# Kernel tuning notes

Hardware: AMD Instinct MI355X
Metric: run time of the kernel (lower is better)

The kernel has to match this reference:

```python
import jax, jax.numpy as jnp
import numpy as np

NUM_HEADS = 8
NUM_LEVELS = 4
NUM_POINTS = 4
EMBED = 256
HEAD_DIM = EMBED // NUM_HEADS
SPATIAL = [(100, 100), (50, 50), (25, 25), (13, 13)]  # (H, W) per level


def _bilinear_sample(val, grid):
    """torch.nn.functional.grid_sample(mode='bilinear', padding_mode='zeros', align_corners=False).
    val: [B, H, W, C], grid: [B, N, 2] with (x, y) in [-1, 1]. Returns [B, N, C]."""
    B, H, W, C = val.shape
    x = (grid[..., 0] + 1.0) * (W * 0.5) - 0.5
    y = (grid[..., 1] + 1.0) * (H * 0.5) - 0.5
    x0 = jnp.floor(x)
    y0 = jnp.floor(y)
    wx1 = x - x0
    wy1 = y - y0
    wx0 = 1.0 - wx1
    wy0 = 1.0 - wy1
    x0i = x0.astype(jnp.int32)
    y0i = y0.astype(jnp.int32)
    valf = val.reshape(B, H * W, C)

    def corner(xi, yi, w):
        valid = (xi >= 0) & (xi < W) & (yi >= 0) & (yi < H)
        idx = jnp.clip(yi, 0, H - 1) * W + jnp.clip(xi, 0, W - 1)
        v = jnp.take_along_axis(valf, idx[..., None], axis=1)  # [B, N, C]
        return v * (w * valid)[..., None]

    return (corner(x0i, y0i, wx0 * wy0) + corner(x0i + 1, y0i, wx1 * wy0)
            + corner(x0i, y0i + 1, wx0 * wy1) + corner(x0i + 1, y0i + 1, wx1 * wy1))


def setup_inputs() -> dict:
    key = jax.random.key(0)
    ks = jax.random.split(key, 12)
    bs, nq = 4, 6000
    nv = sum(h * w for h, w in SPATIAL)
    s = 0.02
    return {
        "query": jax.random.normal(ks[0], (bs, nq, EMBED), jnp.float32),
        "value": jax.random.normal(ks[1], (bs, nv, EMBED), jnp.float32),
        "reference_points": jax.random.uniform(ks[2], (bs, nq, NUM_LEVELS, 2), jnp.float32),
        "W_off": jax.random.normal(ks[3], (EMBED, NUM_HEADS * NUM_LEVELS * NUM_POINTS * 2), jnp.float32) * s,
        "b_off": jax.random.normal(ks[4], (NUM_HEADS * NUM_LEVELS * NUM_POINTS * 2,), jnp.float32),
        "W_attn": jax.random.normal(ks[5], (EMBED, NUM_HEADS * NUM_LEVELS * NUM_POINTS), jnp.float32) * s,
        "b_attn": jnp.zeros((NUM_HEADS * NUM_LEVELS * NUM_POINTS,), jnp.float32),
        "W_val": jax.random.normal(ks[6], (EMBED, EMBED), jnp.float32) * s,
        "b_val": jnp.zeros((EMBED,), jnp.float32),
        "W_out": jax.random.normal(ks[7], (EMBED, EMBED), jnp.float32) * s,
        "b_out": jnp.zeros((EMBED,), jnp.float32),
        "spatial_shapes": jnp.asarray(np.array(SPATIAL, dtype=np.int32)),
    }


def reference(query, value, reference_points, W_off, b_off, W_attn, b_attn,
              W_val, b_val, W_out, b_out, spatial_shapes):
    shapes = [(int(h), int(w)) for h, w in np.asarray(spatial_shapes)]
    bs, nq, _ = query.shape
    nv = value.shape[1]

    v = (value @ W_val + b_val).reshape(bs, nv, NUM_HEADS, HEAD_DIM)
    offsets = (query @ W_off + b_off).reshape(bs, nq, NUM_HEADS, NUM_LEVELS, NUM_POINTS, 2)
    aw = (query @ W_attn + b_attn).reshape(bs, nq, NUM_HEADS, NUM_LEVELS * NUM_POINTS)
    aw = jax.nn.softmax(aw, axis=-1).reshape(bs, nq, NUM_HEADS, NUM_LEVELS, NUM_POINTS)

    # offset normalizer is [W, H] per level
    norm = jnp.asarray([[w, h] for h, w in shapes], dtype=query.dtype)  # [L, 2]
    loc = reference_points[:, :, None, :, None, :] + offsets / norm[None, None, None, :, None, :]
    grids = 2.0 * loc - 1.0  # [bs, nq, H, L, P, 2]
    # -> [bs*H, nq*P, 2] per level
    grids = jnp.transpose(grids, (0, 2, 1, 3, 4, 5)).reshape(bs * NUM_HEADS, nq, NUM_LEVELS, NUM_POINTS, 2)

    v_bh = jnp.transpose(v, (0, 2, 1, 3)).reshape(bs * NUM_HEADS, nv, HEAD_DIM)
    sampled = []
    start = 0
    for l, (H_, W_) in enumerate(shapes):
        val_l = v_bh[:, start:start + H_ * W_].reshape(bs * NUM_HEADS, H_, W_, HEAD_DIM)
        grid_l = grids[:, :, l].reshape(bs * NUM_HEADS, nq * NUM_POINTS, 2)
        s_l = _bilinear_sample(val_l, grid_l).reshape(bs * NUM_HEADS, nq, NUM_POINTS, HEAD_DIM)
        sampled.append(s_l)
        start += H_ * W_
    sampled = jnp.stack(sampled, axis=2)  # [bs*H, nq, L, P, c]

    aw_bh = jnp.transpose(aw, (0, 2, 1, 3, 4)).reshape(bs * NUM_HEADS, nq, NUM_LEVELS, NUM_POINTS)
    out = (sampled * aw_bh[..., None]).sum(axis=(2, 3))  # [bs*H, nq, c]
    out = out.reshape(bs, NUM_HEADS, nq, HEAD_DIM).transpose(0, 2, 1, 3).reshape(bs, nq, EMBED)
    out = out @ W_out + b_out
    return out + query
```

## Files before the change

### kernel.cpp

```cpp
#include <hip/hip_runtime.h>
#include <hip/hip_bf16.h>

#define BS 4
#define NQ 6000
#define NV 13294
#define NH 8
#define HD 32
#define EMB 256
#define MV (BS * NV)
#define MQ (BS * NQ)

typedef __attribute__((ext_vector_type(8))) short short8;
typedef __attribute__((ext_vector_type(4))) float floatx4;

__device__ __constant__ float LVL_DIM[4] = {100.f, 50.f, 25.f, 13.f};

__device__ inline unsigned short bf16bits(float f) {
  __hip_bfloat16 h = __float2bfloat16(f);
  return *reinterpret_cast<unsigned short*>(&h);
}
__device__ inline float bflo(unsigned int u) { return __uint_as_float(u << 16); }
__device__ inline float bfhi(unsigned int u) { return __uint_as_float(u & 0xffff0000u); }

#define LDS_STRIDE 40

__global__ __launch_bounds__(256) void wtrans_kernel(
    const float* __restrict__ W_val, const float* __restrict__ W_off,
    const float* __restrict__ W_attn, const float* __restrict__ W_out,
    unsigned short* __restrict__ Wt_val, unsigned short* __restrict__ Wt_qcat,
    unsigned short* __restrict__ Wt_out) {
  const int b = blockIdx.x, k = threadIdx.x;
  if (b < 256) {
    Wt_val[b * EMB + k] = bf16bits(W_val[k * 256 + b]);
  } else if (b < 640) {
    const int n = b - 256;
    float v = (n < 256) ? W_off[k * 256 + n] : W_attn[k * 128 + (n - 256)];
    Wt_qcat[n * EMB + k] = bf16bits(v);
  } else {
    const int n = b - 640;
    Wt_out[n * EMB + k] = bf16bits(W_out[k * 256 + n]);
  }
}

__device__ inline void stageA_f32(const float* __restrict__ A, int M, int m0,
                                  int k0, unsigned short* lds, int tid) {
  const int r = tid >> 1, half = tid & 1;
  const int row = m0 + r;
  unsigned short* dst = lds + r * LDS_STRIDE + half * 16;
  if (row < M) {
    const float* src = A + (size_t)row * EMB + k0 + half * 16;
#pragma unroll
    for (int j = 0; j < 4; ++j) {
      float4 v = *(const float4*)(src + 4 * j);
      ushort4 u;
      u.x = bf16bits(v.x);
      u.y = bf16bits(v.y);
      u.z = bf16bits(v.z);
      u.w = bf16bits(v.w);
      *(ushort4*)(dst + 4 * j) = u;
    }
  } else {
    ushort4 z = make_ushort4(0, 0, 0, 0);
#pragma unroll
    for (int j = 0; j < 4; ++j) *(ushort4*)(dst + 4 * j) = z;
  }
}

__device__ inline void stage_bf16(const unsigned short* __restrict__ B, int M,
                                  int n0, int k0, unsigned short* lds, int tid) {
  const int r = tid >> 1, half = tid & 1;
  const int row = n0 + r;
  unsigned short* dst = lds + r * LDS_STRIDE + half * 16;
  if (row < M) {
    const unsigned short* src = B + (size_t)row * EMB + k0 + half * 16;
    uint4 v0 = *(const uint4*)(src);
    uint4 v1 = *(const uint4*)(src + 8);
    *(uint4*)(dst) = v0;
    *(uint4*)(dst + 8) = v1;
  } else {
    uint4 z = make_uint4(0, 0, 0, 0);
    *(uint4*)(dst) = z;
    *(uint4*)(dst + 8) = z;
  }
}

__device__ inline void mfma_step(const unsigned short* ldsA,
                                 const unsigned short* ldsB, int wm, int wn,
                                 int lane, floatx4 acc[4][4]) {
  const unsigned short* ap =
      ldsA + (wm * 64 + (lane & 15)) * LDS_STRIDE + (lane >> 4) * 8;
  const unsigned short* bp =
      ldsB + (wn * 64 + (lane & 15)) * LDS_STRIDE + (lane >> 4) * 8;
  short8 af[4], bfr[4];
#pragma unroll
  for (int t = 0; t < 4; ++t) {
    af[t] = *(const short8*)(ap + t * 16 * LDS_STRIDE);
    bfr[t] = *(const short8*)(bp + t * 16 * LDS_STRIDE);
  }
#pragma unroll
  for (int mt = 0; mt < 4; ++mt)
#pragma unroll
    for (int nt = 0; nt < 4; ++nt)
      acc[mt][nt] = __builtin_amdgcn_mfma_f32_16x16x32_bf16(af[mt], bfr[nt],
                                                            acc[mt][nt], 0, 0, 0);
}

__global__ __launch_bounds__(256) void vproj_kernel(
    const float* __restrict__ value, const unsigned short* __restrict__ Wt,
    const float* __restrict__ b_val, unsigned short* __restrict__ vbh) {
  __shared__ unsigned short ldsA[128 * LDS_STRIDE];
  __shared__ unsigned short ldsB[128 * LDS_STRIDE];
  const int tid = threadIdx.x, lane = tid & 63, w = tid >> 6;
  const int wm = w >> 1, wn = w & 1;
  const int chunk = blockIdx.x >> 4, i = blockIdx.x & 15;
  const int m0 = (chunk * 8 + (i & 7)) * 128;
  const int n0 = (i >> 3) * 128;
  floatx4 acc[4][4];
  const floatx4 zero = {0.f, 0.f, 0.f, 0.f};
#pragma unroll
  for (int i2 = 0; i2 < 4; i2++)
#pragma unroll
    for (int j = 0; j < 4; j++) acc[i2][j] = zero;

  for (int k0 = 0; k0 < EMB; k0 += 32) {
    stageA_f32(value, MV, m0, k0, ldsA, tid);
    stage_bf16(Wt, 256, n0, k0, ldsB, tid);
    __syncthreads();
    mfma_step(ldsA, ldsB, wm, wn, lane, acc);
    __syncthreads();
  }

  const int quad = lane >> 4, cl = lane & 15;
#pragma unroll
  for (int mt = 0; mt < 4; ++mt) {
#pragma unroll
    for (int r = 0; r < 4; ++r) {
      const int row = m0 + wm * 64 + mt * 16 + quad * 4 + r;
      if (row < MV) {
        const int b = row / NV, n = row - b * NV;
#pragma unroll
        for (int nt = 0; nt < 4; ++nt) {
          const int c = n0 + wn * 64 + nt * 16 + cl;
          const int h = c >> 5, d = c & 31;
          vbh[(((size_t)(b * NH + h)) * NV + n) * HD + d] =
              bf16bits(acc[mt][nt][r] + b_val[c]);
        }
      }
    }
  }
}

__global__ __launch_bounds__(256) void qproj_kernel(
    const float* __restrict__ query, const unsigned short* __restrict__ Wt,
    const float* __restrict__ refpts, const float* __restrict__ b_off,
    const float* __restrict__ b_attn, float* __restrict__ locbuf,
    float* __restrict__ awbuf) {
  __shared__ unsigned short ldsA[128 * LDS_STRIDE];
  __shared__ unsigned short ldsB[128 * LDS_STRIDE];
  const int tid = threadIdx.x, lane = tid & 63, w = tid >> 6;
  const int wm = w >> 1, wn = w & 1;
  const int chunk = blockIdx.x / 24, i = blockIdx.x % 24;
  const int m_idx = chunk * 8 + (i & 7);
  if (m_idx >= 188) return;
  const int m0 = m_idx * 128;
  const int n0 = (i >> 3) * 128;
  floatx4 acc[4][4];
  const floatx4 zero = {0.f, 0.f, 0.f, 0.f};
#pragma unroll
  for (int i2 = 0; i2 < 4; i2++)
#pragma unroll
    for (int j = 0; j < 4; j++) acc[i2][j] = zero;

  for (int k0 = 0; k0 < EMB; k0 += 32) {
    stageA_f32(query, MQ, m0, k0, ldsA, tid);
    stage_bf16(Wt, 384, n0, k0, ldsB, tid);
    __syncthreads();
    mfma_step(ldsA, ldsB, wm, wn, lane, acc);
    __syncthreads();
  }

  const int quad = lane >> 4, cl = lane & 15;
  if (n0 < 256) {
#pragma unroll
    for (int mt = 0; mt < 4; ++mt) {
#pragma unroll
      for (int r = 0; r < 4; ++r) {
        const int row = m0 + wm * 64 + mt * 16 + quad * 4 + r;
        if (row < MQ) {
#pragma unroll
          for (int nt = 0; nt < 4; ++nt) {
            const int c = n0 + wn * 64 + nt * 16 + cl;
            const int xy = c & 1, l = (c >> 3) & 3;
            const float dim = LVL_DIM[l];
            const float ref = refpts[(size_t)row * 8 + l * 2 + xy];
            locbuf[(size_t)row * 256 + c] =
                ref * dim + acc[mt][nt][r] + b_off[c] - 0.5f;
          }
        }
      }
    }
  } else {
#pragma unroll
    for (int mt = 0; mt < 4; ++mt) {
#pragma unroll
      for (int r = 0; r < 4; ++r) {
        const int row = m0 + wm * 64 + mt * 16 + quad * 4 + r;
        if (row < MQ) {
#pragma unroll
          for (int nt = 0; nt < 4; ++nt) {
            const int ca = wn * 64 + nt * 16 + cl;
            float v = acc[mt][nt][r] + b_attn[ca];
            float m = v;
            m = fmaxf(m, __shfl_xor(m, 1));
            m = fmaxf(m, __shfl_xor(m, 2));
            m = fmaxf(m, __shfl_xor(m, 4));
            m = fmaxf(m, __shfl_xor(m, 8));
            float e = __expf(v - m);
            float s = e;
            s += __shfl_xor(s, 1);
            s += __shfl_xor(s, 2);
            s += __shfl_xor(s, 4);
            s += __shfl_xor(s, 8);
            awbuf[(size_t)row * 128 + ca] = e / s;
          }
        }
      }
    }
  }
}

__global__ __launch_bounds__(256) void sample_kernel(
    const unsigned short* __restrict__ vbh, const float* __restrict__ locbuf,
    const float* __restrict__ awbuf, unsigned short* __restrict__ sampledb) {
  const int blk = blockIdx.x;
  const int t = blk >> 3;
  const int quarter = t / 1500;
  const int j = t - quarter * 1500;
  const int slice = (blk & 7) * 4 + quarter;
  const int h = slice & 7;
  const int w = threadIdx.x >> 6;
  const int lane = threadIdx.x & 63;
  const int row = (slice >> 3) * NQ + j * 4 + w;
  const int g = lane >> 2;
  const int d8 = lane & 3;
  const int l = g >> 2;

  const int W_ = (l < 2) ? ((l == 0) ? 100 : 50) : ((l == 2) ? 25 : 13);
  const int START = (l < 2) ? ((l == 0) ? 0 : 10000) : ((l == 2) ? 12500 : 13125);

  const float2 xy = *(const float2*)(locbuf + (size_t)row * 256 + h * 32 + g * 2);
  const float wgt = awbuf[(size_t)row * 128 + h * 16 + g];

  const float fx = floorf(xy.x), fy = floorf(xy.y);
  const int x0 = (int)fx, y0 = (int)fy;
  const float wx1 = xy.x - fx, wy1 = xy.y - fy;
  const float wx0 = 1.f - wx1, wy0 = 1.f - wy1;
  const int x0c = min(max(x0, 0), W_ - 1), x1c = min(max(x0 + 1, 0), W_ - 1);
  const int y0c = min(max(y0, 0), W_ - 1), y1c = min(max(y0 + 1, 0), W_ - 1);
  const float mx0 = ((unsigned)x0 < (unsigned)W_) ? wx0 : 0.f;
  const float mx1 = ((unsigned)(x0 + 1) < (unsigned)W_) ? wx1 : 0.f;
  const float my0 = ((unsigned)y0 < (unsigned)W_) ? wy0 : 0.f;
  const float my1 = ((unsigned)(y0 + 1) < (unsigned)W_) ? wy1 : 0.f;
  const float wy0w = wgt * my0, wy1w = wgt * my1;
  const float w00 = wy0w * mx0, w01 = wy0w * mx1;
  const float w10 = wy1w * mx0, w11 = wy1w * mx1;

  const unsigned int* base =
      (const unsigned int*)vbh + ((size_t)slice * NV + START) * 16 + d8 * 4;
  const int rb0 = y0c * W_, rb1 = y1c * W_;
  const uint4 u00 = *(const uint4*)(base + (size_t)(rb0 + x0c) * 16);
  const uint4 u01 = *(const uint4*)(base + (size_t)(rb0 + x1c) * 16);
  const uint4 u10 = *(const uint4*)(base + (size_t)(rb1 + x0c) * 16);
  const uint4 u11 = *(const uint4*)(base + (size_t)(rb1 + x1c) * 16);

  float a[8];
  const unsigned int* p00 = &u00.x;
  const unsigned int* p01 = &u01.x;
  const unsigned int* p10 = &u10.x;
  const unsigned int* p11 = &u11.x;
#pragma unroll
  for (int k = 0; k < 4; ++k) {
    a[2 * k] = w00 * bflo(p00[k]) + w01 * bflo(p01[k]) + w10 * bflo(p10[k]) +
               w11 * bflo(p11[k]);
    a[2 * k + 1] = w00 * bfhi(p00[k]) + w01 * bfhi(p01[k]) +
                   w10 * bfhi(p10[k]) + w11 * bfhi(p11[k]);
  }

#pragma unroll
  for (int k = 0; k < 8; ++k) {
    a[k] += __shfl_xor(a[k], 4);
    a[k] += __shfl_xor(a[k], 8);
    a[k] += __shfl_xor(a[k], 16);
    a[k] += __shfl_xor(a[k], 32);
  }

  if (g == 0) {
    uint4 o;
    o.x = (unsigned)bf16bits(a[0]) | ((unsigned)bf16bits(a[1]) << 16);
    o.y = (unsigned)bf16bits(a[2]) | ((unsigned)bf16bits(a[3]) << 16);
    o.z = (unsigned)bf16bits(a[4]) | ((unsigned)bf16bits(a[5]) << 16);
    o.w = (unsigned)bf16bits(a[6]) | ((unsigned)bf16bits(a[7]) << 16);
    *(uint4*)(sampledb + (size_t)row * EMB + h * 32 + d8 * 8) = o;
  }
}

__global__ __launch_bounds__(256) void oproj_kernel(
    const unsigned short* __restrict__ sampledb,
    const unsigned short* __restrict__ Wt, const float* __restrict__ b_out,
    const float* __restrict__ query, float* __restrict__ out) {
  __shared__ unsigned short ldsA[128 * LDS_STRIDE];
  __shared__ unsigned short ldsB[128 * LDS_STRIDE];
  const int tid = threadIdx.x, lane = tid & 63, w = tid >> 6;
  const int wm = w >> 1, wn = w & 1;
  const int chunk = blockIdx.x >> 4, i = blockIdx.x & 15;
  const int m_idx = chunk * 8 + (i & 7);
  if (m_idx >= 188) return;
  const int m0 = m_idx * 128;
  const int n0 = (i >> 3) * 128;
  floatx4 acc[4][4];
  const floatx4 zero = {0.f, 0.f, 0.f, 0.f};
#pragma unroll
  for (int i2 = 0; i2 < 4; i2++)
#pragma unroll
    for (int j = 0; j < 4; j++) acc[i2][j] = zero;

  for (int k0 = 0; k0 < EMB; k0 += 32) {
    stage_bf16(sampledb, MQ, m0, k0, ldsA, tid);
    stage_bf16(Wt, 256, n0, k0, ldsB, tid);
    __syncthreads();
    mfma_step(ldsA, ldsB, wm, wn, lane, acc);
    __syncthreads();
  }

  const int quad = lane >> 4, cl = lane & 15;
#pragma unroll
  for (int mt = 0; mt < 4; ++mt) {
#pragma unroll
    for (int r = 0; r < 4; ++r) {
      const int row = m0 + wm * 64 + mt * 16 + quad * 4 + r;
      if (row < MQ) {
#pragma unroll
        for (int nt = 0; nt < 4; ++nt) {
          const int c = n0 + wn * 64 + nt * 16 + cl;
          out[(size_t)row * EMB + c] =
              acc[mt][nt][r] + b_out[c] + query[(size_t)row * EMB + c];
        }
      }
    }
  }
}

extern "C" void kernel_launch(void* const* d_in, const int* in_sizes, int n_in,
                              void* d_out, int out_size, void* d_ws,
                              size_t ws_size, hipStream_t stream) {
  const float* query  = (const float*)d_in[0];
  const float* value  = (const float*)d_in[1];
  const float* refpts = (const float*)d_in[2];
  const float* W_off  = (const float*)d_in[3];
  const float* b_off  = (const float*)d_in[4];
  const float* W_attn = (const float*)d_in[5];
  const float* b_attn = (const float*)d_in[6];
  const float* W_val  = (const float*)d_in[7];
  const float* b_val  = (const float*)d_in[8];
  const float* W_out  = (const float*)d_in[9];
  const float* b_out  = (const float*)d_in[10];
  float* out = (float*)d_out;

  char* ws = (char*)d_ws;
  unsigned short* vbh = (unsigned short*)ws;
  float* locbuf = (float*)(ws + 27226112);
  float* awbuf = (float*)(ws + 51802112);
  unsigned short* sampledb = (unsigned short*)(ws + 64090112);
  unsigned short* Wt_val = (unsigned short*)(ws + 76378112);
  unsigned short* Wt_qcat = (unsigned short*)(ws + 76509184);
  unsigned short* Wt_out = (unsigned short*)(ws + 76705792);

  wtrans_kernel<<<896, 256, 0, stream>>>(W_val, W_off, W_attn, W_out, Wt_val,
                                         Wt_qcat, Wt_out);
  vproj_kernel<<<832, 256, 0, stream>>>(value, Wt_val, b_val, vbh);
  qproj_kernel<<<576, 256, 0, stream>>>(query, Wt_qcat, refpts, b_off, b_attn,
                                        locbuf, awbuf);
  sample_kernel<<<BS * NQ * NH / 4, 256, 0, stream>>>(vbh, locbuf, awbuf,
                                                      sampledb);
  oproj_kernel<<<384, 256, 0, stream>>>(sampledb, Wt_out, b_out, query, out);
}
```

Measured before the change: 262.5 us.

## Prefetch GEMM tiles into registers, merge value/query projections, pack sampling FMAs

The GEMM main loops now load the next K tile from global memory into registers while the MFMAs run on the current LDS tile, so global latency overlaps with compute. The value and query projection kernels are merged into one launch with 1408 blocks, which cuts one launch and lets both GEMMs share the GPU at once. The bilinear sampling inner loop is rewritten with 2-wide float vectors so the compiler can emit packed FMAs. Holding the prefetched tiles in registers raises register pressure, which may lower occupancy.

```diff
diff --git a/kernel.cpp b/kernel.cpp
--- a/kernel.cpp
+++ b/kernel.cpp
@@ -12,6 +12,7 @@
 
 typedef __attribute__((ext_vector_type(8))) short short8;
 typedef __attribute__((ext_vector_type(4))) float floatx4;
+typedef __attribute__((ext_vector_type(2))) float floatx2;
 
 __device__ __constant__ float LVL_DIM[4] = {100.f, 50.f, 25.f, 13.f};
 
@@ -21,6 +22,12 @@
 }
 __device__ inline float bflo(unsigned int u) { return __uint_as_float(u << 16); }
 __device__ inline float bfhi(unsigned int u) { return __uint_as_float(u & 0xffff0000u); }
+__device__ inline floatx2 unpk(unsigned int u) {
+  floatx2 r;
+  r.x = __uint_as_float(u << 16);
+  r.y = __uint_as_float(u & 0xffff0000u);
+  return r;
+}
 
 #define LDS_STRIDE 40
 
@@ -42,46 +49,51 @@
   }
 }
 
-__device__ inline void stageA_f32(const float* __restrict__ A, int M, int m0,
-                                  int k0, unsigned short* lds, int tid) {
+__device__ inline void loadA_f32(const float* __restrict__ A, int M, int m0,
+                                 int k0, int tid, float4 ra[4]) {
   const int r = tid >> 1, half = tid & 1;
   const int row = m0 + r;
-  unsigned short* dst = lds + r * LDS_STRIDE + half * 16;
   if (row < M) {
     const float* src = A + (size_t)row * EMB + k0 + half * 16;
 #pragma unroll
-    for (int j = 0; j < 4; ++j) {
-      float4 v = *(const float4*)(src + 4 * j);
-      ushort4 u;
-      u.x = bf16bits(v.x);
-      u.y = bf16bits(v.y);
-      u.z = bf16bits(v.z);
-      u.w = bf16bits(v.w);
-      *(ushort4*)(dst + 4 * j) = u;
-    }
+    for (int j = 0; j < 4; ++j) ra[j] = *(const float4*)(src + 4 * j);
   } else {
-    ushort4 z = make_ushort4(0, 0, 0, 0);
-#pragma unroll
-    for (int j = 0; j < 4; ++j) *(ushort4*)(dst + 4 * j) = z;
-  }
-}
-
-__device__ inline void stage_bf16(const unsigned short* __restrict__ B, int M,
-                                  int n0, int k0, unsigned short* lds, int tid) {
+#pragma unroll
+    for (int j = 0; j < 4; ++j) ra[j] = make_float4(0.f, 0.f, 0.f, 0.f);
+  }
+}
+__device__ inline void storeA_lds(unsigned short* lds, int tid,
+                                  const float4 ra[4]) {
+  const int r = tid >> 1, half = tid & 1;
+  unsigned short* dst = lds + r * LDS_STRIDE + half * 16;
+#pragma unroll
+  for (int j = 0; j < 4; ++j) {
+    ushort4 u;
+    u.x = bf16bits(ra[j].x);
+    u.y = bf16bits(ra[j].y);
+    u.z = bf16bits(ra[j].z);
+    u.w = bf16bits(ra[j].w);
+    *(ushort4*)(dst + 4 * j) = u;
+  }
+}
+__device__ inline void loadB_bf16(const unsigned short* __restrict__ B, int M,
+                                  int n0, int k0, int tid, uint4 rb[2]) {
   const int r = tid >> 1, half = tid & 1;
   const int row = n0 + r;
-  unsigned short* dst = lds + r * LDS_STRIDE + half * 16;
   if (row < M) {
     const unsigned short* src = B + (size_t)row * EMB + k0 + half * 16;
-    uint4 v0 = *(const uint4*)(src);
-    uint4 v1 = *(const uint4*)(src + 8);
-    *(uint4*)(dst) = v0;
-    *(uint4*)(dst + 8) = v1;
+    rb[0] = *(const uint4*)(src);
+    rb[1] = *(const uint4*)(src + 8);
   } else {
-    uint4 z = make_uint4(0, 0, 0, 0);
-    *(uint4*)(dst) = z;
-    *(uint4*)(dst + 8) = z;
-  }
+    rb[0] = rb[1] = make_uint4(0, 0, 0, 0);
+  }
+}
+__device__ inline void storeB_lds(unsigned short* lds, int tid,
+                                  const uint4 rb[2]) {
+  const int r = tid >> 1, half = tid & 1;
+  unsigned short* dst = lds + r * LDS_STRIDE + half * 16;
+  *(uint4*)(dst) = rb[0];
+  *(uint4*)(dst + 8) = rb[1];
 }
 
 __device__ inline void mfma_step(const unsigned short* ldsA,
@@ -105,53 +117,56 @@
                                                             acc[mt][nt], 0, 0, 0);
 }
 
-__global__ __launch_bounds__(256) void vproj_kernel(
-    const float* __restrict__ value, const unsigned short* __restrict__ Wt,
-    const float* __restrict__ b_val, unsigned short* __restrict__ vbh) {
-  __shared__ unsigned short ldsA[128 * LDS_STRIDE];
-  __shared__ unsigned short ldsB[128 * LDS_STRIDE];
-  const int tid = threadIdx.x, lane = tid & 63, w = tid >> 6;
-  const int wm = w >> 1, wn = w & 1;
-  const int chunk = blockIdx.x >> 4, i = blockIdx.x & 15;
-  const int m0 = (chunk * 8 + (i & 7)) * 128;
-  const int n0 = (i >> 3) * 128;
-  floatx4 acc[4][4];
-  const floatx4 zero = {0.f, 0.f, 0.f, 0.f};
-#pragma unroll
-  for (int i2 = 0; i2 < 4; i2++)
-#pragma unroll
-    for (int j = 0; j < 4; j++) acc[i2][j] = zero;
-
-  for (int k0 = 0; k0 < EMB; k0 += 32) {
-    stageA_f32(value, MV, m0, k0, ldsA, tid);
-    stage_bf16(Wt, 256, n0, k0, ldsB, tid);
+__device__ inline void gemm_loop_f32A(const float* __restrict__ A, int M,
+                                      int m0, const unsigned short* __restrict__ B,
+                                      int NB, int n0, unsigned short* ldsA,
+                                      unsigned short* ldsB, int tid, int wm,
+                                      int wn, int lane, floatx4 acc[4][4]) {
+  float4 ra[4];
+  uint4 rb[2];
+  loadA_f32(A, M, m0, 0, tid, ra);
+  loadB_bf16(B, NB, n0, 0, tid, rb);
+#pragma unroll
+  for (int k = 0; k < 8; ++k) {
+    storeA_lds(ldsA, tid, ra);
+    storeB_lds(ldsB, tid, rb);
     __syncthreads();
+    if (k < 7) {
+      loadA_f32(A, M, m0, (k + 1) * 32, tid, ra);
+      loadB_bf16(B, NB, n0, (k + 1) * 32, tid, rb);
+    }
     mfma_step(ldsA, ldsB, wm, wn, lane, acc);
     __syncthreads();
   }
-
-  const int quad = lane >> 4, cl = lane & 15;
-#pragma unroll
-  for (int mt = 0; mt < 4; ++mt) {
-#pragma unroll
-    for (int r = 0; r < 4; ++r) {
-      const int row = m0 + wm * 64 + mt * 16 + quad * 4 + r;
-      if (row < MV) {
-        const int b = row / NV, n = row - b * NV;
-#pragma unroll
-        for (int nt = 0; nt < 4; ++nt) {
-          const int c = n0 + wn * 64 + nt * 16 + cl;
-          const int h = c >> 5, d = c & 31;
-          vbh[(((size_t)(b * NH + h)) * NV + n) * HD + d] =
-              bf16bits(acc[mt][nt][r] + b_val[c]);
-        }
-      }
+}
+
+__device__ inline void gemm_loop_bf16A(const unsigned short* __restrict__ A,
+                                       int M, int m0,
+                                       const unsigned short* __restrict__ B,
+                                       int NB, int n0, unsigned short* ldsA,
+                                       unsigned short* ldsB, int tid, int wm,
+                                       int wn, int lane, floatx4 acc[4][4]) {
+  uint4 ra[2], rb[2];
+  loadB_bf16(A, M, m0, 0, tid, ra);
+  loadB_bf16(B, NB, n0, 0, tid, rb);
+#pragma unroll
+  for (int k = 0; k < 8; ++k) {
+    storeB_lds(ldsA, tid, ra);
+    storeB_lds(ldsB, tid, rb);
+    __syncthreads();
+    if (k < 7) {
+      loadB_bf16(A, M, m0, (k + 1) * 32, tid, ra);
+      loadB_bf16(B, NB, n0, (k + 1) * 32, tid, rb);
     }
-  }
-}
-
-__global__ __launch_bounds__(256) void qproj_kernel(
-    const float* __restrict__ query, const unsigned short* __restrict__ Wt,
+    mfma_step(ldsA, ldsB, wm, wn, lane, acc);
+    __syncthreads();
+  }
+}
+
+__global__ __launch_bounds__(256) void vqproj_kernel(
+    const float* __restrict__ value, const unsigned short* __restrict__ Wt_val,
+    const float* __restrict__ b_val, unsigned short* __restrict__ vbh,
+    const float* __restrict__ query, const unsigned short* __restrict__ Wt_qcat,
     const float* __restrict__ refpts, const float* __restrict__ b_off,
     const float* __restrict__ b_attn, float* __restrict__ locbuf,
     float* __restrict__ awbuf) {
@@ -159,69 +174,89 @@
   __shared__ unsigned short ldsB[128 * LDS_STRIDE];
   const int tid = threadIdx.x, lane = tid & 63, w = tid >> 6;
   const int wm = w >> 1, wn = w & 1;
-  const int chunk = blockIdx.x / 24, i = blockIdx.x % 24;
-  const int m_idx = chunk * 8 + (i & 7);
-  if (m_idx >= 188) return;
-  const int m0 = m_idx * 128;
-  const int n0 = (i >> 3) * 128;
   floatx4 acc[4][4];
   const floatx4 zero = {0.f, 0.f, 0.f, 0.f};
 #pragma unroll
   for (int i2 = 0; i2 < 4; i2++)
 #pragma unroll
     for (int j = 0; j < 4; j++) acc[i2][j] = zero;
-
-  for (int k0 = 0; k0 < EMB; k0 += 32) {
-    stageA_f32(query, MQ, m0, k0, ldsA, tid);
-    stage_bf16(Wt, 384, n0, k0, ldsB, tid);
-    __syncthreads();
-    mfma_step(ldsA, ldsB, wm, wn, lane, acc);
-    __syncthreads();
-  }
-
   const int quad = lane >> 4, cl = lane & 15;
-  if (n0 < 256) {
+
+  if (blockIdx.x < 832) {
+    const int chunk = blockIdx.x >> 4, i = blockIdx.x & 15;
+    const int m0 = (chunk * 8 + (i & 7)) * 128;
+    const int n0 = (i >> 3) * 128;
+    gemm_loop_f32A(value, MV, m0, Wt_val, 256, n0, ldsA, ldsB, tid, wm, wn,
+                   lane, acc);
 #pragma unroll
     for (int mt = 0; mt < 4; ++mt) {
 #pragma unroll
       for (int r = 0; r < 4; ++r) {
         const int row = m0 + wm * 64 + mt * 16 + quad * 4 + r;
-        if (row < MQ) {
+        if (row < MV) {
+          const int b = row / NV, n = row - b * NV;
 #pragma unroll
           for (int nt = 0; nt < 4; ++nt) {
             const int c = n0 + wn * 64 + nt * 16 + cl;
-            const int xy = c & 1, l = (c >> 3) & 3;
-            const float dim = LVL_DIM[l];
-            const float ref = refpts[(size_t)row * 8 + l * 2 + xy];
-            locbuf[(size_t)row * 256 + c] =
-                ref * dim + acc[mt][nt][r] + b_off[c] - 0.5f;
+            const int h = c >> 5, d = c & 31;
+            vbh[(((size_t)(b * NH + h)) * NV + n) * HD + d] =
+                bf16bits(acc[mt][nt][r] + b_val[c]);
           }
         }
       }
     }
   } else {
-#pragma unroll
-    for (int mt = 0; mt < 4; ++mt) {
-#pragma unroll
-      for (int r = 0; r < 4; ++r) {
-        const int row = m0 + wm * 64 + mt * 16 + quad * 4 + r;
-        if (row < MQ) {
-#pragma unroll
-          for (int nt = 0; nt < 4; ++nt) {
-            const int ca = wn * 64 + nt * 16 + cl;
-            float v = acc[mt][nt][r] + b_attn[ca];
-            float m = v;
-            m = fmaxf(m, __shfl_xor(m, 1));
-            m = fmaxf(m, __shfl_xor(m, 2));
-            m = fmaxf(m, __shfl_xor(m, 4));
-            m = fmaxf(m, __shfl_xor(m, 8));
-            float e = __expf(v - m);
-            float s = e;
-            s += __shfl_xor(s, 1);
-            s += __shfl_xor(s, 2);
-            s += __shfl_xor(s, 4);
-            s += __shfl_xor(s, 8);
-            awbuf[(size_t)row * 128 + ca] = e / s;
+    const int bid = blockIdx.x - 832;
+    const int chunk = bid / 24, i = bid % 24;
+    const int m_idx = chunk * 8 + (i & 7);
+    if (m_idx >= 188) return;
+    const int m0 = m_idx * 128;
+    const int n0 = (i >> 3) * 128;
+    gemm_loop_f32A(query, MQ, m0, Wt_qcat, 384, n0, ldsA, ldsB, tid, wm, wn,
+                   lane, acc);
+    if (n0 < 256) {
+#pragma unroll
+      for (int mt = 0; mt < 4; ++mt) {
+#pragma unroll
+        for (int r = 0; r < 4; ++r) {
+          const int row = m0 + wm * 64 + mt * 16 + quad * 4 + r;
+          if (row < MQ) {
+#pragma unroll
+            for (int nt = 0; nt < 4; ++nt) {
+              const int c = n0 + wn * 64 + nt * 16 + cl;
+              const int xy = c & 1, l = (c >> 3) & 3;
+              const float dim = LVL_DIM[l];
+              const float ref = refpts[(size_t)row * 8 + l * 2 + xy];
+              locbuf[(size_t)row * 256 + c] =
+                  ref * dim + acc[mt][nt][r] + b_off[c] - 0.5f;
+            }
+          }
+        }
+      }
+    } else {
+#pragma unroll
+      for (int mt = 0; mt < 4; ++mt) {
+#pragma unroll
+        for (int r = 0; r < 4; ++r) {
+          const int row = m0 + wm * 64 + mt * 16 + quad * 4 + r;
+          if (row < MQ) {
+#pragma unroll
+            for (int nt = 0; nt < 4; ++nt) {
+              const int ca = wn * 64 + nt * 16 + cl;
+              float v = acc[mt][nt][r] + b_attn[ca];
+              float m = v;
+              m = fmaxf(m, __shfl_xor(m, 1));
+              m = fmaxf(m, __shfl_xor(m, 2));
+              m = fmaxf(m, __shfl_xor(m, 4));
+              m = fmaxf(m, __shfl_xor(m, 8));
+              float e = __expf(v - m);
+              float s = e;
+              s += __shfl_xor(s, 1);
+              s += __shfl_xor(s, 2);
+              s += __shfl_xor(s, 4);
+              s += __shfl_xor(s, 8);
+              awbuf[(size_t)row * 128 + ca] = e / s;
+            }
           }
         }
       }
@@ -264,6 +299,8 @@
   const float wy0w = wgt * my0, wy1w = wgt * my1;
   const float w00 = wy0w * mx0, w01 = wy0w * mx1;
   const float w10 = wy1w * mx0, w11 = wy1w * mx1;
+  floatx2 w00v = {w00, w00}, w01v = {w01, w01};
+  floatx2 w10v = {w10, w10}, w11v = {w11, w11};
 
   const unsigned int* base =
       (const unsigned int*)vbh + ((size_t)slice * NV + START) * 16 + d8 * 4;
@@ -273,19 +310,26 @@
   const uint4 u10 = *(const uint4*)(base + (size_t)(rb1 + x0c) * 16);
   const uint4 u11 = *(const uint4*)(base + (size_t)(rb1 + x1c) * 16);
 
-  float a[8];
   const unsigned int* p00 = &u00.x;
   const unsigned int* p01 = &u01.x;
   const unsigned int* p10 = &u10.x;
   const unsigned int* p11 = &u11.x;
+  floatx2 a2[4];
 #pragma unroll
   for (int k = 0; k < 4; ++k) {
-    a[2 * k] = w00 * bflo(p00[k]) + w01 * bflo(p01[k]) + w10 * bflo(p10[k]) +
-               w11 * bflo(p11[k]);
-    a[2 * k + 1] = w00 * bfhi(p00[k]) + w01 * bfhi(p01[k]) +
-                   w10 * bfhi(p10[k]) + w11 * bfhi(p11[k]);
-  }
-
+    floatx2 s = w00v * unpk(p00[k]);
+    s += w01v * unpk(p01[k]);
+    s += w10v * unpk(p10[k]);
+    s += w11v * unpk(p11[k]);
+    a2[k] = s;
+  }
+
+  float a[8];
+#pragma unroll
+  for (int k = 0; k < 4; ++k) {
+    a[2 * k] = a2[k].x;
+    a[2 * k + 1] = a2[k].y;
+  }
 #pragma unroll
   for (int k = 0; k < 8; ++k) {
     a[k] += __shfl_xor(a[k], 4);
@@ -324,13 +368,8 @@
 #pragma unroll
     for (int j = 0; j < 4; j++) acc[i2][j] = zero;
 
-  for (int k0 = 0; k0 < EMB; k0 += 32) {
-    stage_bf16(sampledb, MQ, m0, k0, ldsA, tid);
-    stage_bf16(Wt, 256, n0, k0, ldsB, tid);
-    __syncthreads();
-    mfma_step(ldsA, ldsB, wm, wn, lane, acc);
-    __syncthreads();
-  }
+  gemm_loop_bf16A(sampledb, MQ, m0, Wt, 256, n0, ldsA, ldsB, tid, wm, wn, lane,
+                  acc);
 
   const int quad = lane >> 4, cl = lane & 15;
 #pragma unroll
@@ -377,9 +416,9 @@
 
   wtrans_kernel<<<896, 256, 0, stream>>>(W_val, W_off, W_attn, W_out, Wt_val,
                                          Wt_qcat, Wt_out);
-  vproj_kernel<<<832, 256, 0, stream>>>(value, Wt_val, b_val, vbh);
-  qproj_kernel<<<576, 256, 0, stream>>>(query, Wt_qcat, refpts, b_off, b_attn,
-                                        locbuf, awbuf);
+  vqproj_kernel<<<1408, 256, 0, stream>>>(value, Wt_val, b_val, vbh, query,
+                                          Wt_qcat, refpts, b_off, b_attn,
+                                          locbuf, awbuf);
   sample_kernel<<<BS * NQ * NH / 4, 256, 0, stream>>>(vbh, locbuf, awbuf,
                                                       sampledb);
   oproj_kernel<<<384, 256, 0, stream>>>(sampledb, Wt_out, b_out, query, out);
```

Result: no change. 258.8 us (-1.4%).
